# Optimization experiments

Hardware: AMD Instinct MI355X
Metric: run time of the kernel (lower is better)

The kernel has to match this reference:

```python
import jax, jax.numpy as jnp
import numpy as np

DIM = 256
HEADS = 8
DIM_HEAD = 64
SLICE_NUM = 64
INNER = HEADS * DIM_HEAD  # 512
SCALE = DIM_HEAD ** -0.5


def setup_inputs() -> dict:
    key = jax.random.key(0)
    ks = jax.random.split(key, 12)
    b, n = 4, 32768
    s = 0.02
    inp = {
        "x": jax.random.normal(ks[0], (b, n, DIM), dtype=jnp.float32),
        # weights stored as [in, out] so y = x @ W + b
        "W_fx": jax.random.normal(ks[1], (DIM, INNER), dtype=jnp.float32) * s,
        "b_fx": jnp.zeros((INNER,), dtype=jnp.float32),
        "W_x": jax.random.normal(ks[2], (DIM, INNER), dtype=jnp.float32) * s,
        "b_x": jnp.zeros((INNER,), dtype=jnp.float32),
        "W_slice": jax.random.normal(ks[3], (DIM_HEAD, SLICE_NUM), dtype=jnp.float32) * s,
        "b_slice": jnp.zeros((SLICE_NUM,), dtype=jnp.float32),
        "temperature": jnp.ones((1, HEADS, 1, 1), dtype=jnp.float32) * 0.5,
        "Wq": jax.random.normal(ks[4], (DIM_HEAD, DIM_HEAD), dtype=jnp.float32) * s,
        "Wk": jax.random.normal(ks[5], (DIM_HEAD, DIM_HEAD), dtype=jnp.float32) * s,
        "Wv": jax.random.normal(ks[6], (DIM_HEAD, DIM_HEAD), dtype=jnp.float32) * s,
        "W_out": jax.random.normal(ks[7], (INNER, DIM), dtype=jnp.float32) * s,
        "b_out": jnp.zeros((DIM,), dtype=jnp.float32),
    }
    return inp


def reference(x, W_fx, b_fx, W_x, b_x, W_slice, b_slice, temperature,
              Wq, Wk, Wv, W_out, b_out):
    b, n, c = x.shape
    h, d, g = HEADS, DIM_HEAD, SLICE_NUM
    # input projections -> b h n d
    fx_mid = (x @ W_fx + b_fx).reshape(b, n, h, d).transpose(0, 2, 1, 3)
    x_mid = (x @ W_x + b_x).reshape(b, n, h, d).transpose(0, 2, 1, 3)
    # temperature-scaled slice routing softmax: b h n g
    temp = jnp.clip(temperature, 0.1, 5.0)
    slice_logits = (x_mid @ W_slice + b_slice) / temp
    slice_weights = jax.nn.softmax(slice_logits, axis=-1)
    # weighted pooling into slice tokens: b h g d
    slice_tokens = jnp.einsum('bhnc,bhng->bhgc', fx_mid, slice_weights)
    norm = jnp.sum(slice_weights, axis=2)  # b h g
    slice_tokens = slice_tokens / (norm[..., None] + 1e-5)
    # small attention over slice tokens
    q = slice_tokens @ Wq
    k = slice_tokens @ Wk
    v = slice_tokens @ Wv
    attn = jax.nn.softmax(jnp.einsum('bhgd,bhkd->bhgk', q, k) * SCALE, axis=-1)
    out_slice = jnp.einsum('bhgk,bhkd->bhgd', attn, v)
    # scatter back to points: b h n d -> b n (h d)
    out = jnp.einsum('bhgd,bhng->bhnd', out_slice, slice_weights)
    out = out.transpose(0, 2, 1, 3).reshape(b, n, h * d)
    return out @ W_out + b_out
```

## Files before the change

kernel.cpp:

```cpp
#include <hip/hip_runtime.h>
#include <hip/hip_bf16.h>
#include <stdint.h>

#define DIM 256
#define HEADS 8
#define INNER 512
#define NPTS 32768

typedef unsigned int uint32;
typedef short bf16x8 __attribute__((ext_vector_type(8)));
typedef float f32x4 __attribute__((ext_vector_type(4)));

static __device__ __forceinline__ unsigned short f2bf(float f) {
    unsigned int u = __float_as_uint(f);
    u += 0x7fffu + ((u >> 16) & 1u);
    return (unsigned short)(u >> 16);
}
static __device__ __forceinline__ float bf2f(unsigned short v) {
    return __uint_as_float(((unsigned int)v) << 16);
}
static __device__ __forceinline__ uint32 pkbf(float a, float b) {
    __hip_bfloat162 h = __float22bfloat162_rn(make_float2(a, b));
    return *(reinterpret_cast<uint32*>(&h));
}
static __device__ __forceinline__ void gll16(const void* g, const void* l) {
    __builtin_amdgcn_global_load_lds(
        (const __attribute__((address_space(1))) uint32*)g,
        (__attribute__((address_space(3))) uint32*)l, 16, 0, 0);
}

__global__ __launch_bounds__(256) void k_prep(
    const float* __restrict__ Wfx, const float* __restrict__ Wx,
    const float* __restrict__ Wsl,
    unsigned short* __restrict__ Wbt, unsigned short* __restrict__ WslT)
{
    const int blk = blockIdx.x, t = threadIdx.x;
    if (blk < 4) {
        const int n = blk * 256 + t;
        for (int k8 = 0; k8 < 256; k8 += 8) {
            unsigned short v[8];
#pragma unroll
            for (int j = 0; j < 8; j++) {
                float f = (n < 512) ? Wfx[(size_t)(k8 + j) * 512 + n]
                                    : Wx[(size_t)(k8 + j) * 512 + (n - 512)];
                v[j] = f2bf(f);
            }
            ushort4 u0 = {v[0], v[1], v[2], v[3]};
            ushort4 u1 = {v[4], v[5], v[6], v[7]};
            *(ushort4*)(Wbt + (size_t)n * 256 + k8) = u0;
            *(ushort4*)(Wbt + (size_t)n * 256 + k8 + 4) = u1;
        }
    } else {
        const int g = t >> 2, d0 = (t & 3) * 16;
        unsigned short v[16];
#pragma unroll
        for (int i = 0; i < 16; i++) v[i] = f2bf(Wsl[(size_t)(d0 + i) * 64 + g]);
#pragma unroll
        for (int q = 0; q < 4; q++) {
            ushort4 u = {v[q * 4], v[q * 4 + 1], v[q * 4 + 2], v[q * 4 + 3]};
            *(ushort4*)(WslT + (size_t)g * 64 + d0 + q * 4) = u;
        }
    }
}

__global__ __launch_bounds__(256, 2) void k_proj(
    const float* __restrict__ x,
    const unsigned short* __restrict__ Wbt,
    const float* __restrict__ bfx, const float* __restrict__ bx,
    const unsigned short* __restrict__ WslTg,
    const float* __restrict__ bsl, const float* __restrict__ temp,
    unsigned short* __restrict__ fxT,
    unsigned short* __restrict__ wT,
    float* __restrict__ norm)
{
    __shared__ unsigned short R1s[128 * 136];
    __shared__ unsigned short WslS[64 * 64];

    const int ntile = blockIdx.x;
    const int mtile = blockIdx.y;
    const int m0 = mtile * 128;
    const int col0 = ntile * 128;
    const int t = threadIdx.x;
    const int w = t >> 6, lane = t & 63;
    const int wm = w >> 1, wn = w & 1;
    const int l15 = lane & 15, quad = lane >> 4;
    const int b = m0 >> 15;
    const int n_in_b = m0 & (NPTS - 1);

    unsigned short* A = R1s;
    unsigned short* Bs = R1s + 128 * 64;

    if (ntile >= 4) {
        *(uint4*)&WslS[t * 8] = *(const uint4*)&WslTg[t * 8];
        *(uint4*)&WslS[2048 + t * 8] = *(const uint4*)&WslTg[2048 + t * 8];
    }

    f32x4 acc[4][4];
#pragma unroll
    for (int r = 0; r < 4; r++)
#pragma unroll
        for (int c = 0; c < 4; c++) acc[r][c] = (f32x4){0.f, 0.f, 0.f, 0.f};

    for (int kb = 0; kb < 256; kb += 64) {
        float4 a0[4], a1[4];
#pragma unroll
        for (int rr = 0; rr < 4; rr++) {
            int flat = rr * 256 + t;
            int row = flat >> 3, colg = (flat & 7) * 8;
            const float* src = x + (size_t)(m0 + row) * 256 + kb + colg;
            a0[rr] = *(const float4*)src;
            a1[rr] = *(const float4*)(src + 4);
        }
        __syncthreads();
#pragma unroll
        for (int rr = 0; rr < 4; rr++) {
            int flat = rr * 256 + t;
            int row = flat >> 3, colg = (flat & 7) * 8;
            gll16(Wbt + (size_t)(col0 + row) * 256 + kb + colg, (char*)Bs + flat * 16);
        }
#pragma unroll
        for (int rr = 0; rr < 4; rr++) {
            int flat = rr * 256 + t;
            int row = flat >> 3, colg = (flat & 7) * 8;
            uint4 v;
            v.x = pkbf(a0[rr].x, a0[rr].y);
            v.y = pkbf(a0[rr].z, a0[rr].w);
            v.z = pkbf(a1[rr].x, a1[rr].y);
            v.w = pkbf(a1[rr].z, a1[rr].w);
            *(uint4*)&A[row * 64 + colg] = v;
        }
        __syncthreads();
#pragma unroll
        for (int ks = 0; ks < 2; ks++) {
            bf16x8 af[4], bfv[4];
#pragma unroll
            for (int r = 0; r < 4; r++)
                af[r] = *(const bf16x8*)&A[(wm * 64 + r * 16 + l15) * 64 + ks * 32 + quad * 8];
#pragma unroll
            for (int c = 0; c < 4; c++)
                bfv[c] = *(const bf16x8*)&Bs[(wn * 64 + c * 16 + l15) * 64 + ks * 32 + quad * 8];
#pragma unroll
            for (int r = 0; r < 4; r++)
#pragma unroll
                for (int c = 0; c < 4; c++)
                    acc[r][c] = __builtin_amdgcn_mfma_f32_16x16x32_bf16(af[r], bfv[c], acc[r][c], 0, 0, 0);
        }
    }

    if (ntile < 4) {
        float biasc[4];
#pragma unroll
        for (int c = 0; c < 4; c++) biasc[c] = bfx[col0 + wn * 64 + c * 16 + l15];
        __syncthreads();
        unsigned short* fxS = R1s;
#pragma unroll
        for (int r = 0; r < 4; r++)
#pragma unroll
            for (int c = 0; c < 4; c++) {
                ushort4 u;
                u.x = f2bf(acc[r][c][0] + biasc[c]);
                u.y = f2bf(acc[r][c][1] + biasc[c]);
                u.z = f2bf(acc[r][c][2] + biasc[c]);
                u.w = f2bf(acc[r][c][3] + biasc[c]);
                *(ushort4*)&fxS[(wn * 64 + c * 16 + l15) * 136 + wm * 64 + r * 16 + quad * 4] = u;
            }
        __syncthreads();
        const int colL = t >> 1, half = t & 1;
        const int h = (col0 + colL) >> 6, d = (col0 + colL) & 63;
        unsigned short* dst = fxT + (((size_t)(b * 8 + h) * 64 + d) << 15) + n_in_b + half * 64;
        const unsigned short* src = &fxS[colL * 136 + half * 64];
#pragma unroll
        for (int i = 0; i < 8; i++)
            *(uint4*)(dst + i * 8) = *(const uint4*)(src + i * 8);
    } else {
        const int hloc = (ntile - 4) * 2;
        const int head = hloc + wn;
        float biasc[4];
#pragma unroll
        for (int c = 0; c < 4; c++) biasc[c] = bx[(col0 - 512) + wn * 64 + c * 16 + l15];
        __syncthreads();
        unsigned short* xm = R1s;
#pragma unroll
        for (int r = 0; r < 4; r++)
#pragma unroll
            for (int c = 0; c < 4; c++)
#pragma unroll
                for (int j = 0; j < 4; j++)
                    xm[(wm * 64 + r * 16 + quad * 4 + j) * 136 + wn * 64 + c * 16 + l15] =
                        f2bf(acc[r][c][j] + biasc[c]);
        __syncthreads();

        float tv = temp[head];
        tv = fminf(fmaxf(tv, 0.1f), 5.0f);
        const float itemp = 1.0f / tv;

        f32x4 lacc[4][4];
#pragma unroll
        for (int c = 0; c < 4; c++) {
            float bv = bsl[c * 16 + l15];
#pragma unroll
            for (int r = 0; r < 4; r++) lacc[r][c] = (f32x4){bv, bv, bv, bv};
        }
#pragma unroll
        for (int ks = 0; ks < 2; ks++) {
            bf16x8 af[4], bfv[4];
#pragma unroll
            for (int r = 0; r < 4; r++)
                af[r] = *(const bf16x8*)&xm[(wm * 64 + r * 16 + l15) * 136 + wn * 64 + ks * 32 + quad * 8];
#pragma unroll
            for (int c = 0; c < 4; c++)
                bfv[c] = *(const bf16x8*)&WslS[(c * 16 + l15) * 64 + ks * 32 + quad * 8];
#pragma unroll
            for (int r = 0; r < 4; r++)
#pragma unroll
                for (int c = 0; c < 4; c++)
                    lacc[r][c] = __builtin_amdgcn_mfma_f32_16x16x32_bf16(af[r], bfv[c], lacc[r][c], 0, 0, 0);
        }
        __syncthreads();

        unsigned short* wsmT = R1s;
        float ns[4] = {0.f, 0.f, 0.f, 0.f};
#pragma unroll
        for (int r = 0; r < 4; r++) {
            float wv[4][4];
#pragma unroll
            for (int j = 0; j < 4; j++) {
                float v0 = lacc[r][0][j] * itemp;
                float v1 = lacc[r][1][j] * itemp;
                float v2 = lacc[r][2][j] * itemp;
                float v3 = lacc[r][3][j] * itemp;
                float mx = fmaxf(fmaxf(v0, v1), fmaxf(v2, v3));
                mx = fmaxf(mx, __shfl_xor(mx, 1));
                mx = fmaxf(mx, __shfl_xor(mx, 2));
                mx = fmaxf(mx, __shfl_xor(mx, 4));
                mx = fmaxf(mx, __shfl_xor(mx, 8));
                float e0 = __expf(v0 - mx), e1 = __expf(v1 - mx);
                float e2 = __expf(v2 - mx), e3 = __expf(v3 - mx);
                float s = e0 + e1 + e2 + e3;
                s += __shfl_xor(s, 1);
                s += __shfl_xor(s, 2);
                s += __shfl_xor(s, 4);
                s += __shfl_xor(s, 8);
                float inv = 1.0f / s;
                wv[0][j] = e0 * inv; wv[1][j] = e1 * inv;
                wv[2][j] = e2 * inv; wv[3][j] = e3 * inv;
                ns[0] += wv[0][j]; ns[1] += wv[1][j];
                ns[2] += wv[2][j]; ns[3] += wv[3][j];
            }
#pragma unroll
            for (int c = 0; c < 4; c++) {
                ushort4 u;
                u.x = f2bf(wv[c][0]); u.y = f2bf(wv[c][1]);
                u.z = f2bf(wv[c][2]); u.w = f2bf(wv[c][3]);
                *(ushort4*)&wsmT[(wn * 64 + c * 16 + l15) * 136 + wm * 64 + r * 16 + quad * 4] = u;
            }
        }
#pragma unroll
        for (int c = 0; c < 4; c++) {
            ns[c] += __shfl_xor(ns[c], 16);
            ns[c] += __shfl_xor(ns[c], 32);
        }
        if (quad == 0) {
#pragma unroll
            for (int c = 0; c < 4; c++)
                atomicAdd(norm + ((size_t)b * 8 + head) * 64 + c * 16 + l15, ns[c]);
        }
        __syncthreads();
        const int wnn = t >> 7, g = (t >> 1) & 63, half = t & 1;
        const int headg = hloc + wnn;
        unsigned short* dst = wT + (((size_t)(b * 8 + headg) * 64 + g) << 15) + n_in_b + half * 64;
        const unsigned short* src = &wsmT[(wnn * 64 + g) * 136 + half * 64];
#pragma unroll
        for (int i = 0; i < 8; i++)
            *(uint4*)(dst + i * 8) = *(const uint4*)(src + i * 8);
    }
}

#define POOL_SPLIT 16
__global__ __launch_bounds__(256) void k_pool(
    const unsigned short* __restrict__ wT,
    const unsigned short* __restrict__ fxT,
    float* __restrict__ token_num)
{
    __shared__ unsigned short Ap[64 * 64];
    __shared__ unsigned short Bp[64 * 64];
    const int chunk = blockIdx.x, h = blockIdx.y, b = blockIdx.z;
    const int t = threadIdx.x;
    const int w = t >> 6, lane = t & 63, l15 = lane & 15, quad = lane >> 4;
    const size_t base = ((size_t)(b * 8 + h) * 64) << 15;
    const int CH = NPTS / POOL_SPLIT;
    const int n00 = chunk * CH;

    f32x4 acc[4];
#pragma unroll
    for (int c = 0; c < 4; c++) acc[c] = (f32x4){0.f, 0.f, 0.f, 0.f};

    for (int ks0 = 0; ks0 < CH; ks0 += 64) {
        __syncthreads();
#pragma unroll
        for (int rr = 0; rr < 2; rr++) {
            int flat = rr * 256 + t;
            int row = flat >> 3, col = (flat & 7) * 8;
            gll16(wT + base + ((size_t)row << 15) + n00 + ks0 + col, (char*)Ap + flat * 16);
            gll16(fxT + base + ((size_t)row << 15) + n00 + ks0 + col, (char*)Bp + flat * 16);
        }
        __syncthreads();
#pragma unroll
        for (int ks = 0; ks < 2; ks++) {
            bf16x8 af = *(const bf16x8*)&Ap[(w * 16 + l15) * 64 + ks * 32 + quad * 8];
            bf16x8 bfv[4];
#pragma unroll
            for (int c = 0; c < 4; c++)
                bfv[c] = *(const bf16x8*)&Bp[(c * 16 + l15) * 64 + ks * 32 + quad * 8];
#pragma unroll
            for (int c = 0; c < 4; c++)
                acc[c] = __builtin_amdgcn_mfma_f32_16x16x32_bf16(af, bfv[c], acc[c], 0, 0, 0);
        }
    }
    float* tn = token_num + ((size_t)(b * 8 + h) * 64) * 64;
#pragma unroll
    for (int c = 0; c < 4; c++)
#pragma unroll
        for (int j = 0; j < 4; j++)
            atomicAdd(tn + (size_t)(w * 16 + quad * 4 + j) * 64 + c * 16 + l15, acc[c][j]);
}

__global__ __launch_bounds__(256) void k_attn(
    const float* __restrict__ token_num, const float* __restrict__ norm,
    const float* __restrict__ Wq, const float* __restrict__ Wk,
    const float* __restrict__ Wv, float* __restrict__ out_slice)
{
    const int bh = blockIdx.x;
    const int t = threadIdx.x;
    const int gg = t >> 2, qq = t & 3;

    __shared__ float tok[64][68];
    __shared__ float qS[64][68];
    __shared__ float kS[64][68];
    __shared__ float vS[64][68];
    __shared__ float pS[64][68];
    __shared__ float Wqs[64][64], Wks[64][64], Wvs[64][64];

    for (int i = t; i < 4096; i += 256) {
        int g = i >> 6, dd = i & 63;
        Wqs[g][dd] = Wq[i];
        Wks[g][dd] = Wk[i];
        Wvs[g][dd] = Wv[i];
        tok[g][dd] = token_num[(size_t)bh * 4096 + i] / (norm[bh * 64 + g] + 1e-5f);
    }
    __syncthreads();

    float aq[16] = {}, ak[16] = {}, av[16] = {};
    for (int k = 0; k < 64; k++) {
        const float tv = tok[gg][k];
        const float4* wq4 = (const float4*)&Wqs[k][qq * 16];
        const float4* wk4 = (const float4*)&Wks[k][qq * 16];
        const float4* wv4 = (const float4*)&Wvs[k][qq * 16];
#pragma unroll
        for (int j4 = 0; j4 < 4; j4++) {
            float4 a = wq4[j4], bq = wk4[j4], c = wv4[j4];
            aq[j4*4+0] = fmaf(tv, a.x,  aq[j4*4+0]);
            aq[j4*4+1] = fmaf(tv, a.y,  aq[j4*4+1]);
            aq[j4*4+2] = fmaf(tv, a.z,  aq[j4*4+2]);
            aq[j4*4+3] = fmaf(tv, a.w,  aq[j4*4+3]);
            ak[j4*4+0] = fmaf(tv, bq.x, ak[j4*4+0]);
            ak[j4*4+1] = fmaf(tv, bq.y, ak[j4*4+1]);
            ak[j4*4+2] = fmaf(tv, bq.z, ak[j4*4+2]);
            ak[j4*4+3] = fmaf(tv, bq.w, ak[j4*4+3]);
            av[j4*4+0] = fmaf(tv, c.x,  av[j4*4+0]);
            av[j4*4+1] = fmaf(tv, c.y,  av[j4*4+1]);
            av[j4*4+2] = fmaf(tv, c.z,  av[j4*4+2]);
            av[j4*4+3] = fmaf(tv, c.w,  av[j4*4+3]);
        }
    }
#pragma unroll
    for (int j = 0; j < 16; j++) {
        qS[gg][qq * 16 + j] = aq[j];
        kS[gg][qq * 16 + j] = ak[j];
        vS[gg][qq * 16 + j] = av[j];
    }
    __syncthreads();

    float sc[16] = {};
    for (int d4 = 0; d4 < 16; d4++) {
        float4 q4 = *(const float4*)&qS[gg][d4 * 4];
#pragma unroll
        for (int j = 0; j < 16; j++) {
            float4 k4 = *(const float4*)&kS[qq * 16 + j][d4 * 4];
            sc[j] = fmaf(q4.x, k4.x, sc[j]);
            sc[j] = fmaf(q4.y, k4.y, sc[j]);
            sc[j] = fmaf(q4.z, k4.z, sc[j]);
            sc[j] = fmaf(q4.w, k4.w, sc[j]);
        }
    }
    const float SCALE = 0.125f;
    float mx = -1e30f;
#pragma unroll
    for (int j = 0; j < 16; j++) { sc[j] *= SCALE; mx = fmaxf(mx, sc[j]); }
    mx = fmaxf(mx, __shfl_xor(mx, 1));
    mx = fmaxf(mx, __shfl_xor(mx, 2));
    float s = 0.f;
#pragma unroll
    for (int j = 0; j < 16; j++) { sc[j] = __expf(sc[j] - mx); s += sc[j]; }
    s += __shfl_xor(s, 1);
    s += __shfl_xor(s, 2);
    const float invs = 1.0f / s;
#pragma unroll
    for (int j = 0; j < 16; j++) pS[gg][qq * 16 + j] = sc[j] * invs;
    __syncthreads();

    float oo[16] = {};
    for (int j = 0; j < 64; j++) {
        const float pv = pS[gg][j];
        const float4* v4p = (const float4*)&vS[j][qq * 16];
#pragma unroll
        for (int d4 = 0; d4 < 4; d4++) {
            float4 v4 = v4p[d4];
            oo[d4*4+0] = fmaf(pv, v4.x, oo[d4*4+0]);
            oo[d4*4+1] = fmaf(pv, v4.y, oo[d4*4+1]);
            oo[d4*4+2] = fmaf(pv, v4.z, oo[d4*4+2]);
            oo[d4*4+3] = fmaf(pv, v4.w, oo[d4*4+3]);
        }
    }
    float* op = out_slice + (size_t)bh * 4096 + gg * 64 + qq * 16;
#pragma unroll
    for (int d4 = 0; d4 < 4; d4++) {
        float4 o; o.x = oo[d4*4+0]; o.y = oo[d4*4+1]; o.z = oo[d4*4+2]; o.w = oo[d4*4+3];
        *(float4*)(op + d4 * 4) = o;
    }
}

__global__ __launch_bounds__(256) void k_tr(
    const unsigned short* __restrict__ wT, unsigned short* __restrict__ wN)
{
    __shared__ unsigned short tl[64 * 264];
    const int nc = blockIdx.x, h = blockIdx.y, b = blockIdx.z;
    const int t = threadIdx.x;
    const int n0 = nc * 256;
    const size_t base = ((size_t)(b * 8 + h) * 64) << 15;
    {
        const int g = t >> 2, seg = t & 3;
#pragma unroll
        for (int i = 0; i < 8; i++) {
            uint4 v = *(const uint4*)(wT + base + ((size_t)g << 15) + n0 + seg * 64 + i * 8);
            *(uint4*)&tl[g * 264 + seg * 64 + i * 8] = v;
        }
    }
    __syncthreads();
    unsigned short* dst = wN + (size_t)(b * NPTS + n0 + t) * 512 + h * 64;
#pragma unroll
    for (int g4 = 0; g4 < 16; g4++) {
        ushort4 u;
        u.x = tl[(g4 * 4 + 0) * 264 + t];
        u.y = tl[(g4 * 4 + 1) * 264 + t];
        u.z = tl[(g4 * 4 + 2) * 264 + t];
        u.w = tl[(g4 * 4 + 3) * 264 + t];
        *(ushort4*)(dst + g4 * 4) = u;
    }
}

__global__ __launch_bounds__(256) void k_m(
    const float* __restrict__ os, const float* __restrict__ W_out,
    unsigned short* __restrict__ Mt_hi, unsigned short* __restrict__ Mt_lo)
{
    const int h = blockIdx.x, b = blockIdx.y;
    const int t = threadIdx.x;
    __shared__ float osl[64][65];
    for (int i = t; i < 4096; i += 256)
        osl[i >> 6][i & 63] = os[(size_t)(b * 8 + h) * 4096 + i];
    __syncthreads();
    float acc[64];
#pragma unroll
    for (int g = 0; g < 64; g++) acc[g] = 0.f;
    for (int d = 0; d < 64; d++) {
        float wv = W_out[(size_t)(h * 64 + d) * 256 + t];
#pragma unroll
        for (int g = 0; g < 64; g++) acc[g] = fmaf(osl[g][d], wv, acc[g]);
    }
    unsigned short* ph = Mt_hi + (size_t)(b * 256 + t) * 512 + h * 64;
    unsigned short* pl = Mt_lo + (size_t)(b * 256 + t) * 512 + h * 64;
#pragma unroll
    for (int g4 = 0; g4 < 16; g4++) {
        ushort4 uh, ul;
        unsigned short hh; float v, lo;
        v = acc[g4*4+0]; hh = f2bf(v); lo = v - bf2f(hh); uh.x = hh; ul.x = f2bf(lo);
        v = acc[g4*4+1]; hh = f2bf(v); lo = v - bf2f(hh); uh.y = hh; ul.y = f2bf(lo);
        v = acc[g4*4+2]; hh = f2bf(v); lo = v - bf2f(hh); uh.z = hh; ul.z = f2bf(lo);
        v = acc[g4*4+3]; hh = f2bf(v); lo = v - bf2f(hh); uh.w = hh; ul.w = f2bf(lo);
        *(ushort4*)(ph + g4 * 4) = uh;
        *(ushort4*)(pl + g4 * 4) = ul;
    }
}

__global__ __launch_bounds__(256, 2) void k_out(
    const unsigned short* __restrict__ wN,
    const unsigned short* __restrict__ Mt_hi, const unsigned short* __restrict__ Mt_lo,
    const float* __restrict__ bout, float* __restrict__ out)
{
    __shared__ unsigned short A[128 * 64];
    __shared__ unsigned short Bh[128 * 64];
    __shared__ unsigned short Bl[128 * 64];
    const int ntile = blockIdx.x;
    const int mtile = blockIdx.y;
    const int m0 = mtile * 128, col0 = ntile * 128;
    const int b = m0 >> 15;
    const int t = threadIdx.x;
    const int w = t >> 6, lane = t & 63, l15 = lane & 15, quad = lane >> 4;
    const int wm = w >> 1, wn = w & 1;

    f32x4 acc[4][4];
#pragma unroll
    for (int r = 0; r < 4; r++)
#pragma unroll
        for (int c = 0; c < 4; c++) acc[r][c] = (f32x4){0.f, 0.f, 0.f, 0.f};

    for (int kb = 0; kb < 512; kb += 64) {
        __syncthreads();
#pragma unroll
        for (int rr = 0; rr < 4; rr++) {
            int flat = rr * 256 + t;
            int row = flat >> 3, col = (flat & 7) * 8;
            gll16(wN + (size_t)(m0 + row) * 512 + kb + col, (char*)A + flat * 16);
            gll16(Mt_hi + (size_t)(b * 256 + col0 + row) * 512 + kb + col, (char*)Bh + flat * 16);
            gll16(Mt_lo + (size_t)(b * 256 + col0 + row) * 512 + kb + col, (char*)Bl + flat * 16);
        }
        __syncthreads();
#pragma unroll
        for (int ks = 0; ks < 2; ks++) {
            bf16x8 af[4], bh4[4], bl4[4];
#pragma unroll
            for (int r = 0; r < 4; r++)
                af[r] = *(const bf16x8*)&A[(wm * 64 + r * 16 + l15) * 64 + ks * 32 + quad * 8];
#pragma unroll
            for (int c = 0; c < 4; c++) {
                bh4[c] = *(const bf16x8*)&Bh[(wn * 64 + c * 16 + l15) * 64 + ks * 32 + quad * 8];
                bl4[c] = *(const bf16x8*)&Bl[(wn * 64 + c * 16 + l15) * 64 + ks * 32 + quad * 8];
            }
#pragma unroll
            for (int r = 0; r < 4; r++)
#pragma unroll
                for (int c = 0; c < 4; c++) {
                    acc[r][c] = __builtin_amdgcn_mfma_f32_16x16x32_bf16(af[r], bh4[c], acc[r][c], 0, 0, 0);
                    acc[r][c] = __builtin_amdgcn_mfma_f32_16x16x32_bf16(af[r], bl4[c], acc[r][c], 0, 0, 0);
                }
        }
    }
    float biasc[4];
#pragma unroll
    for (int c = 0; c < 4; c++) biasc[c] = bout[col0 + wn * 64 + c * 16 + l15];
#pragma unroll
    for (int r = 0; r < 4; r++)
#pragma unroll
        for (int c = 0; c < 4; c++)
#pragma unroll
            for (int j = 0; j < 4; j++)
                out[(size_t)(m0 + wm * 64 + r * 16 + quad * 4 + j) * 256 + col0 + wn * 64 + c * 16 + l15] =
                    acc[r][c][j] + biasc[c];
}

extern "C" void kernel_launch(void* const* d_in, const int* in_sizes, int n_in,
                              void* d_out, int out_size, void* d_ws, size_t ws_size,
                              hipStream_t stream) {
    const float* x    = (const float*)d_in[0];
    const float* Wfx  = (const float*)d_in[1];
    const float* bfx  = (const float*)d_in[2];
    const float* Wx   = (const float*)d_in[3];
    const float* bx   = (const float*)d_in[4];
    const float* Wsl  = (const float*)d_in[5];
    const float* bsl  = (const float*)d_in[6];
    const float* temp = (const float*)d_in[7];
    const float* Wq   = (const float*)d_in[8];
    const float* Wk   = (const float*)d_in[9];
    const float* Wv   = (const float*)d_in[10];
    const float* Wout = (const float*)d_in[11];
    const float* bout = (const float*)d_in[12];
    float* out = (float*)d_out;

    const int Mtotal = in_sizes[0] / DIM;
    const int B = Mtotal / NPTS;

    char* p = (char*)d_ws;
    unsigned short* Wbt   = (unsigned short*)p; p += (size_t)1024 * 256 * 2;
    unsigned short* WslTg = (unsigned short*)p; p += (size_t)64 * 64 * 2;
    unsigned short* fxT   = (unsigned short*)p; p += (size_t)Mtotal * INNER * 2;
    unsigned short* wT    = (unsigned short*)p; p += (size_t)Mtotal * INNER * 2;
    float* token_num = (float*)p; p += (size_t)B * 8 * 64 * 64 * 4;
    float* norm_ws   = (float*)p; p += (size_t)B * 8 * 64 * 4;
    float* os_ws     = (float*)p; p += (size_t)B * 8 * 64 * 64 * 4;
    unsigned short* Mt_hi = (unsigned short*)p; p += (size_t)B * 256 * 512 * 2;
    unsigned short* Mt_lo = (unsigned short*)p; p += (size_t)B * 256 * 512 * 2;
    unsigned short* wN = fxT;

    hipMemsetAsync(token_num, 0,
                   (size_t)B * 8 * 64 * 64 * 4 + (size_t)B * 8 * 64 * 4, stream);

    k_prep<<<5, 256, 0, stream>>>(Wfx, Wx, Wsl, Wbt, WslTg);
    k_proj<<<dim3(8, Mtotal / 128), 256, 0, stream>>>(
        x, Wbt, bfx, bx, WslTg, bsl, temp, fxT, wT, norm_ws);
    k_pool<<<dim3(POOL_SPLIT, 8, B), 256, 0, stream>>>(wT, fxT, token_num);
    k_attn<<<B * 8, 256, 0, stream>>>(token_num, norm_ws, Wq, Wk, Wv, os_ws);
    k_tr<<<dim3(NPTS / 256, 8, B), 256, 0, stream>>>(wT, wN);
    k_m<<<dim3(8, B), 256, 0, stream>>>(os_ws, Wout, Mt_hi, Mt_lo);
    k_out<<<dim3(2, Mtotal / 128), 256, 0, stream>>>(wN, Mt_hi, Mt_lo, bout, out);
}
```

Measured before the change: 878.3 us.

## Fuse projection, slice softmax, pooling and transpose into one per-head kernel

Each block now handles one head over four 128-point tiles. It computes both the fx and x projections for that head, runs the slice softmax, accumulates pooled slice tokens in registers with MFMA, and writes slice weights directly in point-major layout. This removes the separate pooling and transpose kernels and the round trip of the fxT/wT intermediates through global memory. In exchange, x is re-read once per head (eight times in total instead of per column tile), and occupancy hints for two kernels are raised to three blocks.

```diff
diff --git a/kernel.cpp b/kernel.cpp
--- a/kernel.cpp
+++ b/kernel.cpp
@@ -6,6 +6,8 @@
 #define HEADS 8
 #define INNER 512
 #define NPTS 32768
+#define PADN 136
+#define PADD 72
 
 typedef unsigned int uint32;
 typedef short bf16x8 __attribute__((ext_vector_type(8)));
@@ -63,172 +65,166 @@
     }
 }
 
-__global__ __launch_bounds__(256, 2) void k_proj(
+__global__ __launch_bounds__(256, 3) void k_projfused(
     const float* __restrict__ x,
     const unsigned short* __restrict__ Wbt,
     const float* __restrict__ bfx, const float* __restrict__ bx,
     const unsigned short* __restrict__ WslTg,
     const float* __restrict__ bsl, const float* __restrict__ temp,
-    unsigned short* __restrict__ fxT,
-    unsigned short* __restrict__ wT,
+    unsigned short* __restrict__ wN,
+    float* __restrict__ token_num,
     float* __restrict__ norm)
 {
-    __shared__ unsigned short R1s[128 * 136];
-    __shared__ unsigned short WslS[64 * 64];
-
-    const int ntile = blockIdx.x;
-    const int mtile = blockIdx.y;
-    const int m0 = mtile * 128;
-    const int col0 = ntile * 128;
+    __shared__ unsigned short S[128 * 64 * 2];
+    __shared__ unsigned short X[128 * PADD];
+
+    const int h = blockIdx.x;
+    const int chunk = blockIdx.y;
+    const int b = chunk >> 6;
     const int t = threadIdx.x;
     const int w = t >> 6, lane = t & 63;
     const int wm = w >> 1, wn = w & 1;
     const int l15 = lane & 15, quad = lane >> 4;
-    const int b = m0 >> 15;
-    const int n_in_b = m0 & (NPTS - 1);
-
-    unsigned short* A = R1s;
-    unsigned short* Bs = R1s + 128 * 64;
-
-    if (ntile >= 4) {
-        *(uint4*)&WslS[t * 8] = *(const uint4*)&WslTg[t * 8];
-        *(uint4*)&WslS[2048 + t * 8] = *(const uint4*)&WslTg[2048 + t * 8];
-    }
-
-    f32x4 acc[4][4];
-#pragma unroll
-    for (int r = 0; r < 4; r++)
-#pragma unroll
-        for (int c = 0; c < 4; c++) acc[r][c] = (f32x4){0.f, 0.f, 0.f, 0.f};
-
-    for (int kb = 0; kb < 256; kb += 64) {
-        float4 a0[4], a1[4];
-#pragma unroll
-        for (int rr = 0; rr < 4; rr++) {
-            int flat = rr * 256 + t;
-            int row = flat >> 3, colg = (flat & 7) * 8;
-            const float* src = x + (size_t)(m0 + row) * 256 + kb + colg;
-            a0[rr] = *(const float4*)src;
-            a1[rr] = *(const float4*)(src + 4);
-        }
+
+    unsigned short* A  = S;
+    unsigned short* Bs = S + 128 * 64;
+    unsigned short* fxS = S;
+    unsigned short* wsmT = X;
+
+    bf16x8 wslf[4][2];
+#pragma unroll
+    for (int c = 0; c < 4; c++)
+#pragma unroll
+        for (int ks = 0; ks < 2; ks++)
+            wslf[c][ks] = *(const bf16x8*)&WslTg[(c * 16 + l15) * 64 + ks * 32 + quad * 8];
+
+    float tv = temp[h];
+    tv = fminf(fmaxf(tv, 0.1f), 5.0f);
+    const float itemp = 1.0f / tv;
+    float bsl_c[4], bfx_c[4], bx_c[4];
+#pragma unroll
+    for (int c = 0; c < 4; c++) {
+        bsl_c[c] = bsl[c * 16 + l15];
+        bfx_c[c] = bfx[h * 64 + c * 16 + l15];
+        bx_c[c]  = bx[h * 64 + c * 16 + l15];
+    }
+
+    f32x4 pacc[4];
+#pragma unroll
+    for (int c = 0; c < 4; c++) pacc[c] = (f32x4){0.f, 0.f, 0.f, 0.f};
+    float ns[4] = {0.f, 0.f, 0.f, 0.f};
+
+    for (int mt = 0; mt < 4; mt++) {
+        const int n_in_b = ((chunk & 63) * 4 + mt) * 128;
+        const size_t m0 = (size_t)b * NPTS + n_in_b;
+
+        f32x4 acc[4][4];
+#pragma unroll
+        for (int r = 0; r < 4; r++)
+#pragma unroll
+            for (int c = 0; c < 4; c++) acc[r][c] = (f32x4){0.f, 0.f, 0.f, 0.f};
+
+        for (int kb = 0; kb < 256; kb += 64) {
+            float4 a0[4], a1[4];
+#pragma unroll
+            for (int rr = 0; rr < 4; rr++) {
+                int flat = rr * 256 + t;
+                int row = flat >> 3, colg = (flat & 7) * 8;
+                const float* src = x + (m0 + row) * 256 + kb + colg;
+                a0[rr] = *(const float4*)src;
+                a1[rr] = *(const float4*)(src + 4);
+            }
+            __syncthreads();
+#pragma unroll
+            for (int rr = 0; rr < 4; rr++) {
+                int flat = rr * 256 + t;
+                int row = flat >> 3, colg = (flat & 7) * 8;
+                int grow = (rr < 2) ? (h * 64 + row) : (512 + h * 64 + (row - 64));
+                gll16(Wbt + (size_t)grow * 256 + kb + colg, (char*)Bs + flat * 16);
+            }
+#pragma unroll
+            for (int rr = 0; rr < 4; rr++) {
+                int flat = rr * 256 + t;
+                int row = flat >> 3, colg = (flat & 7) * 8;
+                uint4 v;
+                v.x = pkbf(a0[rr].x, a0[rr].y);
+                v.y = pkbf(a0[rr].z, a0[rr].w);
+                v.z = pkbf(a1[rr].x, a1[rr].y);
+                v.w = pkbf(a1[rr].z, a1[rr].w);
+                *(uint4*)&A[row * 64 + colg] = v;
+            }
+            __syncthreads();
+#pragma unroll
+            for (int ks = 0; ks < 2; ks++) {
+                bf16x8 af[4], bfv[4];
+#pragma unroll
+                for (int r = 0; r < 4; r++)
+                    af[r] = *(const bf16x8*)&A[(wm * 64 + r * 16 + l15) * 64 + ks * 32 + quad * 8];
+#pragma unroll
+                for (int c = 0; c < 4; c++)
+                    bfv[c] = *(const bf16x8*)&Bs[(wn * 64 + c * 16 + l15) * 64 + ks * 32 + quad * 8];
+#pragma unroll
+                for (int r = 0; r < 4; r++)
+#pragma unroll
+                    for (int c = 0; c < 4; c++)
+                        acc[r][c] = __builtin_amdgcn_mfma_f32_16x16x32_bf16(af[r], bfv[c], acc[r][c], 0, 0, 0);
+            }
+        }
+
         __syncthreads();
-#pragma unroll
-        for (int rr = 0; rr < 4; rr++) {
-            int flat = rr * 256 + t;
-            int row = flat >> 3, colg = (flat & 7) * 8;
-            gll16(Wbt + (size_t)(col0 + row) * 256 + kb + colg, (char*)Bs + flat * 16);
-        }
-#pragma unroll
-        for (int rr = 0; rr < 4; rr++) {
-            int flat = rr * 256 + t;
-            int row = flat >> 3, colg = (flat & 7) * 8;
-            uint4 v;
-            v.x = pkbf(a0[rr].x, a0[rr].y);
-            v.y = pkbf(a0[rr].z, a0[rr].w);
-            v.z = pkbf(a1[rr].x, a1[rr].y);
-            v.w = pkbf(a1[rr].z, a1[rr].w);
-            *(uint4*)&A[row * 64 + colg] = v;
+        if (wn == 0) {
+#pragma unroll
+            for (int r = 0; r < 4; r++)
+#pragma unroll
+                for (int c = 0; c < 4; c++) {
+                    ushort4 u;
+                    u.x = f2bf(acc[r][c][0] + bfx_c[c]);
+                    u.y = f2bf(acc[r][c][1] + bfx_c[c]);
+                    u.z = f2bf(acc[r][c][2] + bfx_c[c]);
+                    u.w = f2bf(acc[r][c][3] + bfx_c[c]);
+                    *(ushort4*)&fxS[(c * 16 + l15) * PADN + wm * 64 + r * 16 + quad * 4] = u;
+                }
+        } else {
+#pragma unroll
+            for (int r = 0; r < 4; r++)
+#pragma unroll
+                for (int c = 0; c < 4; c++)
+#pragma unroll
+                    for (int j = 0; j < 4; j++)
+                        X[(wm * 64 + r * 16 + quad * 4 + j) * PADD + c * 16 + l15] =
+                            f2bf(acc[r][c][j] + bx_c[c]);
         }
         __syncthreads();
+
+        f32x4 lacc[2][4];
+#pragma unroll
+        for (int rt = 0; rt < 2; rt++)
+#pragma unroll
+            for (int c = 0; c < 4; c++)
+                lacc[rt][c] = (f32x4){bsl_c[c], bsl_c[c], bsl_c[c], bsl_c[c]};
 #pragma unroll
         for (int ks = 0; ks < 2; ks++) {
-            bf16x8 af[4], bfv[4];
-#pragma unroll
-            for (int r = 0; r < 4; r++)
-                af[r] = *(const bf16x8*)&A[(wm * 64 + r * 16 + l15) * 64 + ks * 32 + quad * 8];
-#pragma unroll
-            for (int c = 0; c < 4; c++)
-                bfv[c] = *(const bf16x8*)&Bs[(wn * 64 + c * 16 + l15) * 64 + ks * 32 + quad * 8];
-#pragma unroll
-            for (int r = 0; r < 4; r++)
+            bf16x8 laf[2];
+#pragma unroll
+            for (int rt = 0; rt < 2; rt++)
+                laf[rt] = *(const bf16x8*)&X[(w * 32 + rt * 16 + l15) * PADD + ks * 32 + quad * 8];
+#pragma unroll
+            for (int rt = 0; rt < 2; rt++)
 #pragma unroll
                 for (int c = 0; c < 4; c++)
-                    acc[r][c] = __builtin_amdgcn_mfma_f32_16x16x32_bf16(af[r], bfv[c], acc[r][c], 0, 0, 0);
-        }
-    }
-
-    if (ntile < 4) {
-        float biasc[4];
-#pragma unroll
-        for (int c = 0; c < 4; c++) biasc[c] = bfx[col0 + wn * 64 + c * 16 + l15];
+                    lacc[rt][c] = __builtin_amdgcn_mfma_f32_16x16x32_bf16(laf[rt], wslf[c][ks], lacc[rt][c], 0, 0, 0);
+        }
         __syncthreads();
-        unsigned short* fxS = R1s;
-#pragma unroll
-        for (int r = 0; r < 4; r++)
-#pragma unroll
-            for (int c = 0; c < 4; c++) {
-                ushort4 u;
-                u.x = f2bf(acc[r][c][0] + biasc[c]);
-                u.y = f2bf(acc[r][c][1] + biasc[c]);
-                u.z = f2bf(acc[r][c][2] + biasc[c]);
-                u.w = f2bf(acc[r][c][3] + biasc[c]);
-                *(ushort4*)&fxS[(wn * 64 + c * 16 + l15) * 136 + wm * 64 + r * 16 + quad * 4] = u;
-            }
-        __syncthreads();
-        const int colL = t >> 1, half = t & 1;
-        const int h = (col0 + colL) >> 6, d = (col0 + colL) & 63;
-        unsigned short* dst = fxT + (((size_t)(b * 8 + h) * 64 + d) << 15) + n_in_b + half * 64;
-        const unsigned short* src = &fxS[colL * 136 + half * 64];
-#pragma unroll
-        for (int i = 0; i < 8; i++)
-            *(uint4*)(dst + i * 8) = *(const uint4*)(src + i * 8);
-    } else {
-        const int hloc = (ntile - 4) * 2;
-        const int head = hloc + wn;
-        float biasc[4];
-#pragma unroll
-        for (int c = 0; c < 4; c++) biasc[c] = bx[(col0 - 512) + wn * 64 + c * 16 + l15];
-        __syncthreads();
-        unsigned short* xm = R1s;
-#pragma unroll
-        for (int r = 0; r < 4; r++)
-#pragma unroll
-            for (int c = 0; c < 4; c++)
-#pragma unroll
-                for (int j = 0; j < 4; j++)
-                    xm[(wm * 64 + r * 16 + quad * 4 + j) * 136 + wn * 64 + c * 16 + l15] =
-                        f2bf(acc[r][c][j] + biasc[c]);
-        __syncthreads();
-
-        float tv = temp[head];
-        tv = fminf(fmaxf(tv, 0.1f), 5.0f);
-        const float itemp = 1.0f / tv;
-
-        f32x4 lacc[4][4];
-#pragma unroll
-        for (int c = 0; c < 4; c++) {
-            float bv = bsl[c * 16 + l15];
-#pragma unroll
-            for (int r = 0; r < 4; r++) lacc[r][c] = (f32x4){bv, bv, bv, bv};
-        }
-#pragma unroll
-        for (int ks = 0; ks < 2; ks++) {
-            bf16x8 af[4], bfv[4];
-#pragma unroll
-            for (int r = 0; r < 4; r++)
-                af[r] = *(const bf16x8*)&xm[(wm * 64 + r * 16 + l15) * 136 + wn * 64 + ks * 32 + quad * 8];
-#pragma unroll
-            for (int c = 0; c < 4; c++)
-                bfv[c] = *(const bf16x8*)&WslS[(c * 16 + l15) * 64 + ks * 32 + quad * 8];
-#pragma unroll
-            for (int r = 0; r < 4; r++)
-#pragma unroll
-                for (int c = 0; c < 4; c++)
-                    lacc[r][c] = __builtin_amdgcn_mfma_f32_16x16x32_bf16(af[r], bfv[c], lacc[r][c], 0, 0, 0);
-        }
-        __syncthreads();
-
-        unsigned short* wsmT = R1s;
-        float ns[4] = {0.f, 0.f, 0.f, 0.f};
-#pragma unroll
-        for (int r = 0; r < 4; r++) {
+
+#pragma unroll
+        for (int rt = 0; rt < 2; rt++) {
             float wv[4][4];
 #pragma unroll
             for (int j = 0; j < 4; j++) {
-                float v0 = lacc[r][0][j] * itemp;
-                float v1 = lacc[r][1][j] * itemp;
-                float v2 = lacc[r][2][j] * itemp;
-                float v3 = lacc[r][3][j] * itemp;
+                float v0 = lacc[rt][0][j] * itemp;
+                float v1 = lacc[rt][1][j] * itemp;
+                float v2 = lacc[rt][2][j] * itemp;
+                float v3 = lacc[rt][3][j] * itemp;
                 float mx = fmaxf(fmaxf(v0, v1), fmaxf(v2, v3));
                 mx = fmaxf(mx, __shfl_xor(mx, 1));
                 mx = fmaxf(mx, __shfl_xor(mx, 2));
@@ -252,77 +248,52 @@
                 ushort4 u;
                 u.x = f2bf(wv[c][0]); u.y = f2bf(wv[c][1]);
                 u.z = f2bf(wv[c][2]); u.w = f2bf(wv[c][3]);
-                *(ushort4*)&wsmT[(wn * 64 + c * 16 + l15) * 136 + wm * 64 + r * 16 + quad * 4] = u;
-            }
-        }
-#pragma unroll
-        for (int c = 0; c < 4; c++) {
-            ns[c] += __shfl_xor(ns[c], 16);
-            ns[c] += __shfl_xor(ns[c], 32);
-        }
-        if (quad == 0) {
-#pragma unroll
-            for (int c = 0; c < 4; c++)
-                atomicAdd(norm + ((size_t)b * 8 + head) * 64 + c * 16 + l15, ns[c]);
+                *(ushort4*)&wsmT[(c * 16 + l15) * PADN + w * 32 + rt * 16 + quad * 4] = u;
+            }
         }
         __syncthreads();
-        const int wnn = t >> 7, g = (t >> 1) & 63, half = t & 1;
-        const int headg = hloc + wnn;
-        unsigned short* dst = wT + (((size_t)(b * 8 + headg) * 64 + g) << 15) + n_in_b + half * 64;
-        const unsigned short* src = &wsmT[(wnn * 64 + g) * 136 + half * 64];
-#pragma unroll
-        for (int i = 0; i < 8; i++)
-            *(uint4*)(dst + i * 8) = *(const uint4*)(src + i * 8);
-    }
-}
-
-#define POOL_SPLIT 16
-__global__ __launch_bounds__(256) void k_pool(
-    const unsigned short* __restrict__ wT,
-    const unsigned short* __restrict__ fxT,
-    float* __restrict__ token_num)
-{
-    __shared__ unsigned short Ap[64 * 64];
-    __shared__ unsigned short Bp[64 * 64];
-    const int chunk = blockIdx.x, h = blockIdx.y, b = blockIdx.z;
-    const int t = threadIdx.x;
-    const int w = t >> 6, lane = t & 63, l15 = lane & 15, quad = lane >> 4;
-    const size_t base = ((size_t)(b * 8 + h) * 64) << 15;
-    const int CH = NPTS / POOL_SPLIT;
-    const int n00 = chunk * CH;
-
-    f32x4 acc[4];
-#pragma unroll
-    for (int c = 0; c < 4; c++) acc[c] = (f32x4){0.f, 0.f, 0.f, 0.f};
-
-    for (int ks0 = 0; ks0 < CH; ks0 += 64) {
-        __syncthreads();
-#pragma unroll
-        for (int rr = 0; rr < 2; rr++) {
-            int flat = rr * 256 + t;
-            int row = flat >> 3, col = (flat & 7) * 8;
-            gll16(wT + base + ((size_t)row << 15) + n00 + ks0 + col, (char*)Ap + flat * 16);
-            gll16(fxT + base + ((size_t)row << 15) + n00 + ks0 + col, (char*)Bp + flat * 16);
-        }
-        __syncthreads();
-#pragma unroll
-        for (int ks = 0; ks < 2; ks++) {
-            bf16x8 af = *(const bf16x8*)&Ap[(w * 16 + l15) * 64 + ks * 32 + quad * 8];
-            bf16x8 bfv[4];
-#pragma unroll
-            for (int c = 0; c < 4; c++)
-                bfv[c] = *(const bf16x8*)&Bp[(c * 16 + l15) * 64 + ks * 32 + quad * 8];
-#pragma unroll
-            for (int c = 0; c < 4; c++)
-                acc[c] = __builtin_amdgcn_mfma_f32_16x16x32_bf16(af, bfv[c], acc[c], 0, 0, 0);
-        }
-    }
+
+#pragma unroll
+        for (int kk = 0; kk < 4; kk++) {
+            bf16x8 paf = *(const bf16x8*)&wsmT[(w * 16 + l15) * PADN + kk * 32 + quad * 8];
+#pragma unroll
+            for (int c = 0; c < 4; c++) {
+                bf16x8 pbf = *(const bf16x8*)&fxS[(c * 16 + l15) * PADN + kk * 32 + quad * 8];
+                pacc[c] = __builtin_amdgcn_mfma_f32_16x16x32_bf16(paf, pbf, pacc[c], 0, 0, 0);
+            }
+        }
+
+        {
+            const int n = t >> 1, half = t & 1;
+            unsigned short* dst = wN + ((size_t)b * NPTS + n_in_b + n) * 512 + h * 64 + half * 32;
+#pragma unroll
+            for (int g4 = 0; g4 < 8; g4++) {
+                ushort4 u;
+                u.x = wsmT[(half * 32 + g4 * 4 + 0) * PADN + n];
+                u.y = wsmT[(half * 32 + g4 * 4 + 1) * PADN + n];
+                u.z = wsmT[(half * 32 + g4 * 4 + 2) * PADN + n];
+                u.w = wsmT[(half * 32 + g4 * 4 + 3) * PADN + n];
+                *(ushort4*)(dst + g4 * 4) = u;
+            }
+        }
+    }
+
     float* tn = token_num + ((size_t)(b * 8 + h) * 64) * 64;
 #pragma unroll
     for (int c = 0; c < 4; c++)
 #pragma unroll
         for (int j = 0; j < 4; j++)
-            atomicAdd(tn + (size_t)(w * 16 + quad * 4 + j) * 64 + c * 16 + l15, acc[c][j]);
+            atomicAdd(tn + (size_t)(w * 16 + quad * 4 + j) * 64 + c * 16 + l15, pacc[c][j]);
+#pragma unroll
+    for (int c = 0; c < 4; c++) {
+        ns[c] += __shfl_xor(ns[c], 16);
+        ns[c] += __shfl_xor(ns[c], 32);
+    }
+    if (quad == 0) {
+#pragma unroll
+        for (int c = 0; c < 4; c++)
+            atomicAdd(norm + ((size_t)b * 8 + h) * 64 + c * 16 + l15, ns[c]);
+    }
 }
 
 __global__ __launch_bounds__(256) void k_attn(
@@ -430,35 +401,6 @@
     }
 }
 
-__global__ __launch_bounds__(256) void k_tr(
-    const unsigned short* __restrict__ wT, unsigned short* __restrict__ wN)
-{
-    __shared__ unsigned short tl[64 * 264];
-    const int nc = blockIdx.x, h = blockIdx.y, b = blockIdx.z;
-    const int t = threadIdx.x;
-    const int n0 = nc * 256;
-    const size_t base = ((size_t)(b * 8 + h) * 64) << 15;
-    {
-        const int g = t >> 2, seg = t & 3;
-#pragma unroll
-        for (int i = 0; i < 8; i++) {
-            uint4 v = *(const uint4*)(wT + base + ((size_t)g << 15) + n0 + seg * 64 + i * 8);
-            *(uint4*)&tl[g * 264 + seg * 64 + i * 8] = v;
-        }
-    }
-    __syncthreads();
-    unsigned short* dst = wN + (size_t)(b * NPTS + n0 + t) * 512 + h * 64;
-#pragma unroll
-    for (int g4 = 0; g4 < 16; g4++) {
-        ushort4 u;
-        u.x = tl[(g4 * 4 + 0) * 264 + t];
-        u.y = tl[(g4 * 4 + 1) * 264 + t];
-        u.z = tl[(g4 * 4 + 2) * 264 + t];
-        u.w = tl[(g4 * 4 + 3) * 264 + t];
-        *(ushort4*)(dst + g4 * 4) = u;
-    }
-}
-
 __global__ __launch_bounds__(256) void k_m(
     const float* __restrict__ os, const float* __restrict__ W_out,
     unsigned short* __restrict__ Mt_hi, unsigned short* __restrict__ Mt_lo)
@@ -492,7 +434,7 @@
     }
 }
 
-__global__ __launch_bounds__(256, 2) void k_out(
+__global__ __launch_bounds__(256, 3) void k_out(
     const unsigned short* __restrict__ wN,
     const unsigned short* __restrict__ Mt_hi, const unsigned short* __restrict__ Mt_lo,
     const float* __restrict__ bout, float* __restrict__ out)
@@ -582,24 +524,20 @@
     char* p = (char*)d_ws;
     unsigned short* Wbt   = (unsigned short*)p; p += (size_t)1024 * 256 * 2;
     unsigned short* WslTg = (unsigned short*)p; p += (size_t)64 * 64 * 2;
-    unsigned short* fxT   = (unsigned short*)p; p += (size_t)Mtotal * INNER * 2;
-    unsigned short* wT    = (unsigned short*)p; p += (size_t)Mtotal * INNER * 2;
+    unsigned short* wN    = (unsigned short*)p; p += (size_t)Mtotal * INNER * 2;
     float* token_num = (float*)p; p += (size_t)B * 8 * 64 * 64 * 4;
     float* norm_ws   = (float*)p; p += (size_t)B * 8 * 64 * 4;
     float* os_ws     = (float*)p; p += (size_t)B * 8 * 64 * 64 * 4;
     unsigned short* Mt_hi = (unsigned short*)p; p += (size_t)B * 256 * 512 * 2;
     unsigned short* Mt_lo = (unsigned short*)p; p += (size_t)B * 256 * 512 * 2;
-    unsigned short* wN = fxT;
 
     hipMemsetAsync(token_num, 0,
                    (size_t)B * 8 * 64 * 64 * 4 + (size_t)B * 8 * 64 * 4, stream);
 
     k_prep<<<5, 256, 0, stream>>>(Wfx, Wx, Wsl, Wbt, WslTg);
-    k_proj<<<dim3(8, Mtotal / 128), 256, 0, stream>>>(
-        x, Wbt, bfx, bx, WslTg, bsl, temp, fxT, wT, norm_ws);
-    k_pool<<<dim3(POOL_SPLIT, 8, B), 256, 0, stream>>>(wT, fxT, token_num);
+    k_projfused<<<dim3(8, (Mtotal / 128) / 4), 256, 0, stream>>>(
+        x, Wbt, bfx, bx, WslTg, bsl, temp, wN, token_num, norm_ws);
     k_attn<<<B * 8, 256, 0, stream>>>(token_num, norm_ws, Wq, Wk, Wv, os_ws);
-    k_tr<<<dim3(NPTS / 256, 8, B), 256, 0, stream>>>(wT, wN);
     k_m<<<dim3(8, B), 256, 0, stream>>>(os_ws, Wout, Mt_hi, Mt_lo);
     k_out<<<dim3(2, Mtotal / 128), 256, 0, stream>>>(wN, Mt_hi, Mt_lo, bout, out);
 }
```

After: 840.2 us. 4.3% less time.
